# Performance work log

Hardware: AMD Instinct MI355X
Metric: run time of the kernel (lower is better)

## Reference

```python
import jax, jax.numpy as jnp
import numpy as np

N_NODES = 100_000
N_EDGES = 6_400_000  # avg degree 64
ONE_THIRD = 1.0 / 3.0


def _safe_cbrt(x):
    # x >= 0 by construction (relu upstream); guard x==0 so pow grad stays finite.
    pos = x > 0
    xs = jnp.where(pos, x, 1.0)
    return jnp.where(pos, xs ** ONE_THIRD, 0.0)


def setup_inputs() -> dict:
    key = jax.random.key(0)
    ks = jax.random.split(key, 8)
    T = jax.random.uniform(ks[0], (N_NODES,), jnp.float32, 1.8, 4.5)          # node temperature [K]
    cp = jax.random.uniform(ks[1], (N_NODES,), jnp.float32, 0.5, 2.0)         # node thermal capacity
    L = jax.random.uniform(ks[2], (N_EDGES,), jnp.float32, 0.1, 2.0)          # edge length (>0)
    conductivity = jax.random.uniform(ks[3], (N_EDGES,), jnp.float32, 0.5, 1.5)
    A = jax.random.uniform(ks[4], (N_EDGES,), jnp.float32, 0.01, 1.0)         # cross-section area
    src = jax.random.randint(ks[5], (N_EDGES,), 0, N_NODES, jnp.int32)
    dst = jax.random.randint(ks[6], (N_EDGES,), 0, N_NODES, jnp.int32)
    time_step = jnp.full((1,), 0.1, jnp.float32)                              # context scalar
    return {"T": T, "cp": cp, "L": L, "conductivity": conductivity, "A": A,
            "time_step": time_step, "src": src, "dst": dst}


def reference(T, cp, L, conductivity, A, time_step, src, dst):
    n = T.shape[0]
    # broadcast node -> edge; relu(-(T_target - T_source)) == relu(T_src - T_dst)
    delta_T = jax.nn.relu(T[src] - T[dst])                 # [E]
    gradient_T = delta_T / L                               # [E]
    heat_flux_density = _safe_cbrt(gradient_T * conductivity)
    heat_flux = heat_flux_density * A
    E_transf_conduction = heat_flux * time_step            # broadcast [1]
    cp_s = cp[src]
    cp_t = cp[dst]
    combined_cp = cp_t * cp_s / (cp_t + cp_s)
    max_energy = delta_T * combined_cp
    E_transf = jnp.minimum(E_transf_conduction, max_energy)
    heat_sent = jax.ops.segment_sum(E_transf, src, num_segments=n)
    heat_received = jax.ops.segment_sum(E_transf, dst, num_segments=n)
    return heat_received - heat_sent                       # [N]
```

## Files before the change

kernel.cpp:

```cpp
#include <hip/hip_runtime.h>
#include <hip/hip_bf16.h>
#include <hip/hip_fp16.h>

#define NRANGE   8
#define RLEN_MAX 12800
#define N_XCD    8
#define SL_XCD   8
#define SLICES   64
#define WIN_E    2048

typedef float vfloat4 __attribute__((ext_vector_type(4)));
typedef unsigned long long u64;

__global__ void __launch_bounds__(256)
pack_nodes_kernel(const float* __restrict__ T, const float* __restrict__ cp,
                  float2* __restrict__ nodes, int n) {
    int i = blockIdx.x * blockDim.x + threadIdx.x;
    if (i < n) nodes[i] = make_float2(T[i], cp[i]);
}

__device__ __forceinline__ float edge_e(float2 ns, float2 nd, float Li,
                                        float ci, float Ai, float dt) {
    const float delta = ns.x - nd.x;
    if (delta <= 0.0f) return 0.0f;
    const float x = (delta / Li) * ci;
    const float ec = cbrtf(x) * Ai * dt;
    const float comb = (nd.y * ns.y) / (nd.y + ns.y);
    return fminf(ec, delta * comb);
}

__device__ __forceinline__ u64 make_rec(int s, int d, float e) {
    return (u64)(unsigned)s | ((u64)(unsigned)d << 17)
         | ((u64)__half_as_ushort(__float2half_rn(e)) << 34);
}

__global__ void __launch_bounds__(512)
etrec_kernel(const float2* __restrict__ nodes,
             const float* __restrict__ L,
             const float* __restrict__ cond,
             const float* __restrict__ A,
             const float* __restrict__ time_step,
             const int* __restrict__ src,
             const int* __restrict__ dst,
             u64* __restrict__ recs,
             int* __restrict__ tails,
             int n_edges, int wps, int cap) {
    __shared__ u64 srec[WIN_E];
    __shared__ int scnt, sbase;
    if (threadIdx.x == 0) scnt = 0;
    __syncthreads();

    const int wpx = SL_XCD * wps;
    const int w   = (blockIdx.x % N_XCD) * wpx + blockIdx.x / N_XCD;
    const int s   = w / wps;
    const int e0  = w * WIN_E;

    if (e0 < n_edges) {
        const float dt = time_step[0];
        const int e1 = min(n_edges, e0 + WIN_E);
        const int ng = (e1 - e0) >> 2;
        const int g  = threadIdx.x;
        if (g < ng) {
            const int kk = (e0 >> 2) + g;
            const int4    si = ((const int4*)src)[kk];
            const int4    di = ((const int4*)dst)[kk];
            const vfloat4 Lv = __builtin_nontemporal_load(&((const vfloat4*)L)[kk]);
            const vfloat4 cv = __builtin_nontemporal_load(&((const vfloat4*)cond)[kk]);
            const vfloat4 Av = __builtin_nontemporal_load(&((const vfloat4*)A)[kk]);
            const float2 ns0 = nodes[si.x], ns1 = nodes[si.y], ns2 = nodes[si.z], ns3 = nodes[si.w];
            const float2 nd0 = nodes[di.x], nd1 = nodes[di.y], nd2 = nodes[di.z], nd3 = nodes[di.w];
            const float ex = edge_e(ns0, nd0, Lv.x, cv.x, Av.x, dt);
            const float ey = edge_e(ns1, nd1, Lv.y, cv.y, Av.y, dt);
            const float ez = edge_e(ns2, nd2, Lv.z, cv.z, Av.z, dt);
            const float ew = edge_e(ns3, nd3, Lv.w, cv.w, Av.w, dt);
            if (ex > 0.0f) { int p = atomicAdd(&scnt, 1); srec[p] = make_rec(si.x, di.x, ex); }
            if (ey > 0.0f) { int p = atomicAdd(&scnt, 1); srec[p] = make_rec(si.y, di.y, ey); }
            if (ez > 0.0f) { int p = atomicAdd(&scnt, 1); srec[p] = make_rec(si.z, di.z, ez); }
            if (ew > 0.0f) { int p = atomicAdd(&scnt, 1); srec[p] = make_rec(si.w, di.w, ew); }
        }
        const int tb = e0 + (ng << 2);
        const int ti = tb + g;
        if (ti < e1) {
            const float e = edge_e(nodes[src[ti]], nodes[dst[ti]], L[ti], cond[ti], A[ti], dt);
            if (e > 0.0f) { int p = atomicAdd(&scnt, 1); srec[p] = make_rec(src[ti], dst[ti], e); }
        }
    }
    __syncthreads();
    if (threadIdx.x == 0) sbase = atomicAdd(&tails[s], scnt);
    __syncthreads();
    const int wr = min(scnt, max(0, cap - sbase));
    u64* __restrict__ dp = recs + (size_t)s * cap + sbase;
    for (int t = threadIdx.x; t < wr; t += 512) dp[t] = srec[t];
}

__global__ void __launch_bounds__(512)
accrec_kernel(const u64* __restrict__ recs,
              const int* __restrict__ tails,
              float* __restrict__ copies,
              int n_nodes, int R, int cap) {
    __shared__ float lds[RLEN_MAX];
    const int xcd = blockIdx.x % N_XCD;
    const int j   = blockIdx.x / N_XCD;
    const int r   = j % NRANGE;
    const int b   = xcd * SL_XCD + j / NRANGE;
    const int base = r * R;
    const int rlen = min(R, n_nodes - base);

    for (int t = threadIdx.x; t < rlen; t += 512) lds[t] = 0.0f;
    __syncthreads();

    const int cnt = min(tails[b], cap);
    const u64* __restrict__ g = recs + (size_t)b * cap;
    for (int t = threadIdx.x; t < cnt; t += 512) {
        const u64 rec = g[t];
        const int   sv = (int)(rec & 0x1FFFF);
        const int   dv = (int)((rec >> 17) & 0x1FFFF);
        const float e  = __half2float(__ushort_as_half((unsigned short)(rec >> 34)));
        const int ls = sv - base; if ((unsigned)ls < (unsigned)rlen) atomicAdd(&lds[ls], -e);
        const int ld = dv - base; if ((unsigned)ld < (unsigned)rlen) atomicAdd(&lds[ld],  e);
    }
    __syncthreads();

    float* __restrict__ cpy = copies + (size_t)b * n_nodes + base;
    for (int t = threadIdx.x; t < rlen; t += 512) cpy[t] = lds[t];
}

__global__ void __launch_bounds__(256)
reduce_copies_kernel(const float* __restrict__ copies, float* __restrict__ out,
                     int n_nodes) {
    const int k = blockIdx.x * blockDim.x + threadIdx.x;
    const int nvec = n_nodes >> 2;
    if (k < nvec) {
        vfloat4 v = {0.f, 0.f, 0.f, 0.f};
        for (int b = 0; b < SLICES; ++b)
            v += ((const vfloat4*)(copies + (size_t)b * n_nodes))[k];
        ((vfloat4*)out)[k] = v;
    } else if (k == nvec) {
        for (int i = nvec << 2; i < n_nodes; ++i) {
            float v = 0.0f;
            for (int b = 0; b < SLICES; ++b) v += copies[(size_t)b * n_nodes + i];
            out[i] = v;
        }
    }
}

__global__ void __launch_bounds__(256)
conduction_edge_direct(const float* __restrict__ T, const float* __restrict__ cp,
                       const float* __restrict__ L, const float* __restrict__ cond,
                       const float* __restrict__ A, const float* __restrict__ time_step,
                       const int* __restrict__ src, const int* __restrict__ dst,
                       float* __restrict__ out, int n_edges) {
    int i = blockIdx.x * blockDim.x + threadIdx.x;
    if (i >= n_edges) return;
    const int s = src[i], d = dst[i];
    float delta = T[s] - T[d];
    if (delta <= 0.0f) return;
    const float dt = time_step[0];
    const float x = (delta / L[i]) * cond[i];
    const float e_cond = cbrtf(x) * A[i] * dt;
    const float cs = cp[s], cd = cp[d];
    const float max_e = delta * (cd * cs) / (cd + cs);
    const float Et = fminf(e_cond, max_e);
    atomicAdd(&out[d],  Et);
    atomicAdd(&out[s], -Et);
}

extern "C" void kernel_launch(void* const* d_in, const int* in_sizes, int n_in,
                              void* d_out, int out_size, void* d_ws, size_t ws_size,
                              hipStream_t stream) {
    const float* T    = (const float*)d_in[0];
    const float* cp   = (const float*)d_in[1];
    const float* L    = (const float*)d_in[2];
    const float* cond = (const float*)d_in[3];
    const float* A    = (const float*)d_in[4];
    const float* ts   = (const float*)d_in[5];
    const int*   src  = (const int*)d_in[6];
    const int*   dst  = (const int*)d_in[7];
    float* out = (float*)d_out;

    const int n_nodes = in_sizes[0];
    const int n_edges = in_sizes[2];

    const int block = 256;
    const int ngrid = (n_nodes + block - 1) / block;
    const int R = (n_nodes + NRANGE - 1) / NRANGE;

    int chunk = (n_edges + SLICES - 1) / SLICES;
    chunk = (chunk + WIN_E - 1) & ~(WIN_E - 1);
    const int wps = chunk / WIN_E;
    const int cap = (chunk >> 3) * 5;

    const size_t tails_bytes = 256;
    const size_t nodes_bytes = (size_t)n_nodes * sizeof(float2);
    const size_t recs_bytes  = (size_t)SLICES * cap * sizeof(u64);
    const size_t copy_bytes  = (size_t)SLICES * n_nodes * sizeof(float);
    const size_t need = tails_bytes + nodes_bytes + recs_bytes + copy_bytes;

    if (R <= RLEN_MAX && n_nodes <= (1 << 17) && ws_size >= need) {
        int*    tails  = (int*)d_ws;
        float2* nodes  = (float2*)((char*)d_ws + tails_bytes);
        u64*    recs   = (u64*)((char*)d_ws + tails_bytes + nodes_bytes);
        float*  copies = (float*)((char*)d_ws + tails_bytes + nodes_bytes + recs_bytes);

        (void)hipMemsetAsync(tails, 0, SLICES * sizeof(int), stream);
        pack_nodes_kernel<<<ngrid, block, 0, stream>>>(T, cp, nodes, n_nodes);
        etrec_kernel<<<SLICES * wps, 512, 0, stream>>>(
            nodes, L, cond, A, ts, src, dst, recs, tails, n_edges, wps, cap);
        accrec_kernel<<<N_XCD * SL_XCD * NRANGE, 512, 0, stream>>>(
            recs, tails, copies, n_nodes, R, cap);
        const int rgrid = ((n_nodes >> 2) + 1 + block - 1) / block;
        reduce_copies_kernel<<<rgrid, block, 0, stream>>>(copies, out, n_nodes);
    } else {
        (void)hipMemsetAsync(out, 0, (size_t)out_size * sizeof(float), stream);
        const int egrid = (n_edges + block - 1) / block;
        conduction_edge_direct<<<egrid, block, 0, stream>>>(
            T, cp, L, cond, A, ts, src, dst, out, n_edges);
    }
}
```

Measured before the change: 248.9 us.

## Emit edge records via wave-aggregated global atomics and fold tail reset into pack

Replaces the shared-memory staging buffer and block-level barriers in the edge kernel with per-wavefront ballot-based compaction, where one lane per wave reserves space in the slice's global tail counter and each lane writes its record directly. The tail-counter memset is folded into the node-packing kernel, removing one launch. The slice count is halved to 32, which gives fewer partial copies to reduce but longer slice chunks and a smaller accumulate grid. The change trades LDS staging and barriers for more global atomics on shared tail counters and scattered, less coalesced record writes.

```diff
diff --git a/kernel.cpp b/kernel.cpp
--- a/kernel.cpp
+++ b/kernel.cpp
@@ -5,8 +5,8 @@
 #define NRANGE   8
 #define RLEN_MAX 12800
 #define N_XCD    8
-#define SL_XCD   8
-#define SLICES   64
+#define SL_XCD   4
+#define SLICES   32
 #define WIN_E    2048
 
 typedef float vfloat4 __attribute__((ext_vector_type(4)));
@@ -14,9 +14,10 @@
 
 __global__ void __launch_bounds__(256)
 pack_nodes_kernel(const float* __restrict__ T, const float* __restrict__ cp,
-                  float2* __restrict__ nodes, int n) {
+                  float2* __restrict__ nodes, int* __restrict__ tails, int n) {
     int i = blockIdx.x * blockDim.x + threadIdx.x;
     if (i < n) nodes[i] = make_float2(T[i], cp[i]);
+    if (blockIdx.x == 0 && threadIdx.x < SLICES) tails[threadIdx.x] = 0;
 }
 
 __device__ __forceinline__ float edge_e(float2 ns, float2 nd, float Li,
@@ -32,6 +33,23 @@
 __device__ __forceinline__ u64 make_rec(int s, int d, float e) {
     return (u64)(unsigned)s | ((u64)(unsigned)d << 17)
          | ((u64)__half_as_ushort(__float2half_rn(e)) << 34);
+}
+
+__device__ __forceinline__ void emit_rec(float e, int sv, int dv,
+                                         int* __restrict__ tail,
+                                         u64* __restrict__ dp, int cap) {
+    const u64 mask = __ballot(e > 0.0f);
+    if (mask == 0ull) return;
+    const int lane = threadIdx.x & 63;
+    const int leader = __ffsll((long long)mask) - 1;
+    int base = 0;
+    if (lane == leader) base = atomicAdd(tail, __popcll(mask));
+    base = __shfl(base, leader, 64);
+    if (e > 0.0f) {
+        const int off = __popcll(mask & ((1ull << lane) - 1ull));
+        const int p = base + off;
+        if (p < cap) dp[p] = make_rec(sv, dv, e);
+    }
 }
 
 __global__ void __launch_bounds__(512)
@@ -45,52 +63,46 @@
              u64* __restrict__ recs,
              int* __restrict__ tails,
              int n_edges, int wps, int cap) {
-    __shared__ u64 srec[WIN_E];
-    __shared__ int scnt, sbase;
-    if (threadIdx.x == 0) scnt = 0;
-    __syncthreads();
-
     const int wpx = SL_XCD * wps;
     const int w   = (blockIdx.x % N_XCD) * wpx + blockIdx.x / N_XCD;
     const int s   = w / wps;
     const int e0  = w * WIN_E;
-
-    if (e0 < n_edges) {
-        const float dt = time_step[0];
-        const int e1 = min(n_edges, e0 + WIN_E);
-        const int ng = (e1 - e0) >> 2;
-        const int g  = threadIdx.x;
-        if (g < ng) {
-            const int kk = (e0 >> 2) + g;
-            const int4    si = ((const int4*)src)[kk];
-            const int4    di = ((const int4*)dst)[kk];
-            const vfloat4 Lv = __builtin_nontemporal_load(&((const vfloat4*)L)[kk]);
-            const vfloat4 cv = __builtin_nontemporal_load(&((const vfloat4*)cond)[kk]);
-            const vfloat4 Av = __builtin_nontemporal_load(&((const vfloat4*)A)[kk]);
-            const float2 ns0 = nodes[si.x], ns1 = nodes[si.y], ns2 = nodes[si.z], ns3 = nodes[si.w];
-            const float2 nd0 = nodes[di.x], nd1 = nodes[di.y], nd2 = nodes[di.z], nd3 = nodes[di.w];
-            const float ex = edge_e(ns0, nd0, Lv.x, cv.x, Av.x, dt);
-            const float ey = edge_e(ns1, nd1, Lv.y, cv.y, Av.y, dt);
-            const float ez = edge_e(ns2, nd2, Lv.z, cv.z, Av.z, dt);
-            const float ew = edge_e(ns3, nd3, Lv.w, cv.w, Av.w, dt);
-            if (ex > 0.0f) { int p = atomicAdd(&scnt, 1); srec[p] = make_rec(si.x, di.x, ex); }
-            if (ey > 0.0f) { int p = atomicAdd(&scnt, 1); srec[p] = make_rec(si.y, di.y, ey); }
-            if (ez > 0.0f) { int p = atomicAdd(&scnt, 1); srec[p] = make_rec(si.z, di.z, ez); }
-            if (ew > 0.0f) { int p = atomicAdd(&scnt, 1); srec[p] = make_rec(si.w, di.w, ew); }
-        }
+    if (e0 >= n_edges) return;
+
+    u64* __restrict__ dp = recs + (size_t)s * cap;
+    const float dt = time_step[0];
+    const int e1 = min(n_edges, e0 + WIN_E);
+    const int ng = (e1 - e0) >> 2;
+    const int g  = threadIdx.x;
+
+    if (g < ng) {
+        const int kk = (e0 >> 2) + g;
+        const int4    si = ((const int4*)src)[kk];
+        const int4    di = ((const int4*)dst)[kk];
+        const vfloat4 Lv = __builtin_nontemporal_load(&((const vfloat4*)L)[kk]);
+        const vfloat4 cv = __builtin_nontemporal_load(&((const vfloat4*)cond)[kk]);
+        const vfloat4 Av = __builtin_nontemporal_load(&((const vfloat4*)A)[kk]);
+        const float2 ns0 = nodes[si.x], ns1 = nodes[si.y], ns2 = nodes[si.z], ns3 = nodes[si.w];
+        const float2 nd0 = nodes[di.x], nd1 = nodes[di.y], nd2 = nodes[di.z], nd3 = nodes[di.w];
+        const float ex = edge_e(ns0, nd0, Lv.x, cv.x, Av.x, dt);
+        const float ey = edge_e(ns1, nd1, Lv.y, cv.y, Av.y, dt);
+        const float ez = edge_e(ns2, nd2, Lv.z, cv.z, Av.z, dt);
+        const float ew = edge_e(ns3, nd3, Lv.w, cv.w, Av.w, dt);
+        emit_rec(ex, si.x, di.x, &tails[s], dp, cap);
+        emit_rec(ey, si.y, di.y, &tails[s], dp, cap);
+        emit_rec(ez, si.z, di.z, &tails[s], dp, cap);
+        emit_rec(ew, si.w, di.w, &tails[s], dp, cap);
+    } else {
         const int tb = e0 + (ng << 2);
-        const int ti = tb + g;
+        const int ti = tb + (g - ng);
         if (ti < e1) {
             const float e = edge_e(nodes[src[ti]], nodes[dst[ti]], L[ti], cond[ti], A[ti], dt);
-            if (e > 0.0f) { int p = atomicAdd(&scnt, 1); srec[p] = make_rec(src[ti], dst[ti], e); }
+            if (e > 0.0f) {
+                const int p = atomicAdd(&tails[s], 1);
+                if (p < cap) dp[p] = make_rec(src[ti], dst[ti], e);
+            }
         }
     }
-    __syncthreads();
-    if (threadIdx.x == 0) sbase = atomicAdd(&tails[s], scnt);
-    __syncthreads();
-    const int wr = min(scnt, max(0, cap - sbase));
-    u64* __restrict__ dp = recs + (size_t)s * cap + sbase;
-    for (int t = threadIdx.x; t < wr; t += 512) dp[t] = srec[t];
 }
 
 __global__ void __launch_bounds__(512)
@@ -202,8 +214,7 @@
         u64*    recs   = (u64*)((char*)d_ws + tails_bytes + nodes_bytes);
         float*  copies = (float*)((char*)d_ws + tails_bytes + nodes_bytes + recs_bytes);
 
-        (void)hipMemsetAsync(tails, 0, SLICES * sizeof(int), stream);
-        pack_nodes_kernel<<<ngrid, block, 0, stream>>>(T, cp, nodes, n_nodes);
+        pack_nodes_kernel<<<ngrid, block, 0, stream>>>(T, cp, nodes, tails, n_nodes);
         etrec_kernel<<<SLICES * wps, 512, 0, stream>>>(
             nodes, L, cond, A, ts, src, dst, recs, tails, n_edges, wps, cap);
         accrec_kernel<<<N_XCD * SL_XCD * NRANGE, 512, 0, stream>>>(
```

Result: slower. 780.1 us (+213.5%).
